# Kernel optimization log

Hardware: AMD Instinct MI355X
Metric: run time of the kernel (lower is better)

## Reference

```python
import jax, jax.numpy as jnp
import numpy as np

# --- static config (matches init_kwargs) ---
DIM = 192          # kv channels
CS = 2             # channel_scale -> q/out channels = DIM//CS
NH = 6             # num heads
WS = 4             # kv window size (q window = 2*WS)
S, H, W = 16, 32, 32          # coarse (input) resolution
SD, HD, WD = 32, 64, 64
HEAD = DIM // NH
SCALE = HEAD ** -0.5

# Relative position index: query coords are the fine-grid positions mapped to
# coarse coords via repeat_interleave(2) (as in the original coords_s/h/w),
# key coords are the coarse window positions. (Original torch code contained a
# buggy 2D->3D port of the strided key subsample; this is the consistent 3D form.)
_r = np.repeat(np.arange(WS), 2)
qc = np.stack(np.meshgrid(_r, _r, _r, indexing='ij'), -1).reshape(-1, 3)        # (512,3)
_k = np.arange(WS)
kc = np.stack(np.meshgrid(_k, _k, _k, indexing='ij'), -1).reshape(-1, 3)        # (64,3)
_rel = qc[:, None, :] - kc[None, :, :] + (WS - 1)                                # in [0, 2*WS-2]
REL_INDEX = jnp.asarray(_rel[..., 0] * (2 * WS - 1) ** 2 + _rel[..., 1] * (2 * WS - 1) + _rel[..., 2])  # (512,64)
TABLE_ROWS = (4 * WS - 1) ** 3  # as in original parameter shape


def ln(x, g, b, eps=1e-5):
    mu = jnp.mean(x, axis=-1, keepdims=True)
    var = jnp.mean(jnp.square(x - mu), axis=-1, keepdims=True)
    return (x - mu) * jax.lax.rsqrt(var + eps) * g + b


def win_part(x, ws):
    # (B,s,h,w,C) -> (B*num_windows, ws^3, C)
    B, s, h, w, C = x.shape
    x = x.reshape(B, s // ws, ws, h // ws, ws, w // ws, ws, C)
    return x.transpose(0, 1, 3, 5, 2, 4, 6, 7).reshape(-1, ws * ws * ws, C)


def win_rev(x, ws, B, s, h, w):
    # (B*num_windows, ws^3, C) -> (B,s,h,w,C)
    C = x.shape[-1]
    x = x.reshape(B, s // ws, h // ws, w // ws, ws, ws, ws, C)
    return x.transpose(0, 1, 4, 2, 5, 3, 6, 7).reshape(B, s, h, w, C)


def setup_inputs() -> dict:
    key = jax.random.key(0)
    ks = jax.random.split(key, 12)
    d = DIM
    dh = d // CS
    hid = int(dh * 4)
    f = lambda i, shape: jax.random.normal(ks[i], shape, jnp.float32) * 0.02
    return dict(
        x=jax.random.normal(ks[0], (2, S * H * W, d), jnp.float32),
        x_downsampled=jax.random.normal(ks[1], (2, SD * HD * WD, dh), jnp.float32),
        gamma1=jnp.ones((d,), jnp.float32), beta1=jnp.zeros((d,), jnp.float32),
        W_kv=f(2, (d, 2 * d)), b_kv=jnp.zeros((2 * d,), jnp.float32),
        W_q=f(3, (dh, d)), b_q=jnp.zeros((d,), jnp.float32),
        W_proj=f(4, (d, dh)), b_proj=jnp.zeros((dh,), jnp.float32),
        bias_table=f(5, (TABLE_ROWS, NH)),
        exp_gamma=jnp.ones((d,), jnp.float32), exp_beta=jnp.zeros((d,), jnp.float32),
        deconv_w=f(6, (d, dh, 2, 2, 2)), deconv_b=jnp.zeros((dh,), jnp.float32),
        gamma2=jnp.ones((dh,), jnp.float32), beta2=jnp.zeros((dh,), jnp.float32),
        W1=f(7, (dh, hid)), b1=jnp.zeros((hid,), jnp.float32),
        W2=f(8, (hid, dh)), b2=jnp.zeros((dh,), jnp.float32),
        padwh=0,
    )


def reference(x, x_downsampled, gamma1, beta1, W_kv, b_kv, W_q, b_q, W_proj, b_proj,
              bias_table, exp_gamma, exp_beta, deconv_w, deconv_b, gamma2, beta2,
              W1, b1, W2, b2, padwh):
    B = x.shape[0]
    d = DIM
    dh = d // CS
    # ---- windowed cross attention: kv from coarse x (norm1), q from fine skip ----
    kv = ln(x, gamma1, beta1).reshape(B, S, H, W, d)
    kv_w = win_part(kv, WS)                                           # (Bw, 64, d)
    q_w = win_part(x_downsampled.reshape(B, SD, HD, WD, dh), 2 * WS)  # (Bw, 512, dh)
    Bw, N, _ = kv_w.shape
    Nq = q_w.shape[1]
    kvp = kv_w @ W_kv + b_kv                                          # (Bw, N, 2d)
    k, v = jnp.split(kvp, 2, axis=-1)
    k = k.reshape(Bw, N, NH, HEAD).transpose(0, 2, 1, 3)
    v = v.reshape(Bw, N, NH, HEAD).transpose(0, 2, 1, 3)
    q = (q_w @ W_q + b_q).reshape(Bw, Nq, NH, HEAD).transpose(0, 2, 1, 3) * SCALE
    attn = jnp.einsum('bhqd,bhkd->bhqk', q, k)                        # (Bw, NH, 512, 64)
    bias = bias_table[REL_INDEX].transpose(2, 0, 1)                   # (NH, 512, 64)
    attn = jax.nn.softmax(attn + bias[None], axis=-1)
    out = jnp.einsum('bhqk,bhkd->bhqd', attn, v).transpose(0, 2, 1, 3).reshape(Bw, Nq, d)
    out = out @ W_proj + b_proj                                       # (Bw, Nq, dh)
    out = win_rev(out, 2 * WS, B, SD, HD, WD).reshape(B, SD * HD * WD, dh)
    # ---- Patch_Expanding residual: LN + ConvTranspose3d(k=2, s=2) ----
    xe = ln(x, exp_gamma, exp_beta).reshape(B, S, H, W, d)
    sc = jnp.einsum('bshwc,coijk->bsihjwko', xe, deconv_w) + deconv_b  # (B,S,2,H,2,W,2,dh)
    sc = sc.reshape(B, SD * HD * WD, dh)
    # ---- residual + MLP ----
    y = sc + out
    hdn = jax.nn.gelu(ln(y, gamma2, beta2) @ W1 + b1, approximate=False)
    return y + (hdn @ W2 + b2)
```

## Files before the change

### kernel.cpp

```cpp
#include <hip/hip_runtime.h>
#include <math.h>

#define ATT_SCALE 0.17677669529663687f

typedef __bf16 bf16x8 __attribute__((ext_vector_type(8)));
typedef __bf16 bf16x4 __attribute__((ext_vector_type(4)));
typedef float  f32x4  __attribute__((ext_vector_type(4)));

#define MFMA16(a,b,c) __builtin_amdgcn_mfma_f32_16x16x32_bf16(a,b,c,0,0,0)

#define BIAS_BYTES 786432
#define WKV_OFF 0
#define WQ_OFF  73728
#define WP_OFF  92160
#define WD_OFF  110592
#define W1_OFF  258048
#define W2_OFF  294912
#define NSWZ    331776

static __device__ __forceinline__ float gelu_exact(float v){
    return 0.5f * v * (1.0f + erff(v * 0.70710678118654752f));
}

static __device__ __forceinline__ bf16x8 afrag(const __bf16* w, int NRT, int kt, int rt, int lane){
    return ((const bf16x8*)w)[(kt*NRT + rt)*64 + lane];
}

__global__ __launch_bounds__(256) void k_prep(const float* __restrict__ table,
    const float* __restrict__ Wkv, const float* __restrict__ Wq,
    const float* __restrict__ Wp,  const float* __restrict__ Wd,
    const float* __restrict__ W1,  const float* __restrict__ W2,
    float* __restrict__ bias, __bf16* __restrict__ wsw){
    int id = blockIdx.x * 256 + threadIdx.x;
    if (id < 196608){
        int k  = id & 63;
        int qg = (id >> 6) & 511;
        int h  = id >> 15;
        int qi = qg >> 6, qj = (qg >> 3) & 7, qk = qg & 7;
        int ki = k >> 4,  kj = (k >> 2) & 3,  kk = k & 3;
        int r0 = (qi >> 1) - ki + 3;
        int r1 = (qj >> 1) - kj + 3;
        int r2 = (qk >> 1) - kk + 3;
        bias[id] = table[((r0 * 7 + r1) * 7 + r2) * 6 + h];
        return;
    }
    id -= 196608;
    if (id >= NSWZ) return;
    if (id >= WD_OFF && id < W1_OFF){
        int lid  = id - WD_OFF;
        int j    = lid & 7, lane = (lid >> 3) & 63, tile = lid >> 9;
        int rt   = tile % 24;
        int kt2  = tile / 24;
        int ii   = kt2 / 6, kt = kt2 % 6;
        int n    = rt * 16 + (lane & 15);
        int o    = n % 96, jk = n / 96;
        int kdim = kt * 32 + (lane >> 4) * 8 + j;
        wsw[id] = (__bf16)(Wd[(kdim * 96 + o) * 8 + ii * 4 + jk]);
        return;
    }
    const float* W; int N, NRT, off; float sc = 1.f;
    if      (id < WQ_OFF){ W = Wkv; N = 384; NRT = 24; off = WKV_OFF; }
    else if (id < WP_OFF){ W = Wq;  N = 192; NRT = 12; off = WQ_OFF; sc = ATT_SCALE; }
    else if (id < WD_OFF){ W = Wp;  N = 96;  NRT = 6;  off = WP_OFF; }
    else if (id < W2_OFF){ W = W1;  N = 384; NRT = 24; off = W1_OFF; }
    else                 { W = W2;  N = 96;  NRT = 6;  off = W2_OFF; }
    int lid  = id - off;
    int j    = lid & 7, lane = (lid >> 3) & 63, tile = lid >> 9;
    int rt   = tile % NRT, kt = tile / NRT;
    int n    = rt * 16 + (lane & 15);
    int k    = kt * 32 + (lane >> 4) * 8 + j;
    wsw[id + 0] = (__bf16)(W[k * N + n] * sc);
}

__global__ __launch_bounds__(512) void k_deconv(const float* __restrict__ x,
    const float* __restrict__ eg, const float* __restrict__ eb,
    const __bf16* __restrict__ wsw, const float* __restrict__ db,
    float* __restrict__ out){
    __shared__ __bf16 xe[64][200];
    const int tid = threadIdx.x, lane = tid & 63, w = tid >> 6;
    const int ci0 = blockIdx.x * 64;
    {
        int row = tid >> 3, sub = tid & 7;
        const float* xp = x + (ci0 + row) * 192 + sub * 24;
        float v[24]; float s = 0.f, ss = 0.f;
        #pragma unroll
        for (int i = 0; i < 6; i++){
            float4 t = ((const float4*)xp)[i];
            v[4*i] = t.x; v[4*i+1] = t.y; v[4*i+2] = t.z; v[4*i+3] = t.w;
            s += t.x + t.y + t.z + t.w;
            ss += t.x*t.x + t.y*t.y + t.z*t.z + t.w*t.w;
        }
        #pragma unroll
        for (int m = 1; m < 8; m <<= 1){ s += __shfl_xor(s, m); ss += __shfl_xor(ss, m); }
        float mu = s * (1.f/192.f), var = ss * (1.f/192.f) - mu*mu, rs = rsqrtf(var + 1e-5f);
        #pragma unroll
        for (int i = 0; i < 3; i++){
            bf16x8 t;
            #pragma unroll
            for (int jj = 0; jj < 8; jj++){
                int c = sub*24 + 8*i + jj;
                t[jj] = (__bf16)((v[8*i+jj] - mu) * rs * eg[c] + eb[c]);
            }
            *(bf16x8*)&xe[row][sub*24 + 8*i] = t;
        }
    }
    __syncthreads();
    const int li = lane & 15, gt = lane >> 4;
    const int ct = w & 3, ii = w >> 2;
    const int tok = ct * 16 + li;
    const int ci  = ci0 + tok;
    const int bb  = ci >> 14, rem = ci & 16383;
    const int sC  = rem >> 10, hC = (rem >> 5) & 31, wC = rem & 31;
    const int ftb = ((bb * 32 + 2 * sC) * 64 + 2 * hC) * 64 + 2 * wC + ii * 4096;
    bf16x8 bfr[6];
    #pragma unroll
    for (int kt = 0; kt < 6; kt++) bfr[kt] = *(const bf16x8*)&xe[tok][kt*32 + gt*8];
    const __bf16* wd = wsw + WD_OFF + ii * 73728;
    for (int rt = 0; rt < 24; rt++){
        f32x4 acc = {0.f,0.f,0.f,0.f};
        #pragma unroll
        for (int kt = 0; kt < 6; kt++) acc = MFMA16(afrag(wd, 24, kt, rt, lane), bfr[kt], acc);
        int m  = rt * 16 + (gt << 2);
        int jk = m / 96, o = m - jk * 96;
        int ft = ftb + (jk >> 1) * 64 + (jk & 1);
        float4 d4 = *(const float4*)&db[o];
        float4 res;
        res.x = acc[0] + d4.x; res.y = acc[1] + d4.y;
        res.z = acc[2] + d4.z; res.w = acc[3] + d4.w;
        *(float4*)&out[ft * 96 + o] = res;
    }
}

__global__ __launch_bounds__(512) void k_attn(const float* __restrict__ x,
    const float* __restrict__ xd, const float* __restrict__ g1, const float* __restrict__ b1v,
    const float* __restrict__ bkv, const float* __restrict__ bq, const float* __restrict__ bpj,
    const __bf16* __restrict__ wsw, const float* __restrict__ bias, float* __restrict__ yout){
    __shared__ __bf16 Qs[64][196];
    __shared__ __bf16 Ks[64][196];
    __shared__ __bf16 Vt[192][68];
    const int tid = threadIdx.x, lane = tid & 63, w = tid >> 6;
    const int win = blockIdx.x, b = win >> 8, wrem = win & 255;
    const int sw_ = wrem >> 6, hw_ = (wrem >> 3) & 7, ww_ = wrem & 7;

    {
        int row = tid >> 3, sub = tid & 7;
        int si = row >> 4, hi = (row >> 2) & 3, wi = row & 3;
        int ci = ((b * 16 + 4 * sw_ + si) * 32 + 4 * hw_ + hi) * 32 + 4 * ww_ + wi;
        const float* xp = x + ci * 192 + sub * 24;
        float v[24]; float s = 0.f, ss = 0.f;
        #pragma unroll
        for (int i = 0; i < 6; i++){
            float4 t = ((const float4*)xp)[i];
            v[4*i] = t.x; v[4*i+1] = t.y; v[4*i+2] = t.z; v[4*i+3] = t.w;
            s += t.x + t.y + t.z + t.w;
            ss += t.x*t.x + t.y*t.y + t.z*t.z + t.w*t.w;
        }
        #pragma unroll
        for (int m = 1; m < 8; m <<= 1){ s += __shfl_xor(s, m); ss += __shfl_xor(ss, m); }
        float mu = s * (1.f/192.f), var = ss * (1.f/192.f) - mu*mu, rs = rsqrtf(var + 1e-5f);
        #pragma unroll
        for (int i = 0; i < 3; i++){
            bf16x8 t;
            #pragma unroll
            for (int jj = 0; jj < 8; jj++){
                int c = sub*24 + 8*i + jj;
                t[jj] = (__bf16)((v[8*i+jj] - mu) * rs * g1[c] + b1v[c]);
            }
            *(bf16x8*)&Qs[row][sub*24 + 8*i] = t;
        }
    }
    __syncthreads();
    {
        const int ct = w & 3, rh = w >> 2;
        const int tok = ct * 16 + (lane & 15);
        bf16x8 bfr[6];
        #pragma unroll
        for (int kt = 0; kt < 6; kt++) bfr[kt] = *(const bf16x8*)&Qs[tok][kt*32 + (lane>>4)*8];
        #pragma unroll
        for (int i = 0; i < 12; i++){
            int rt = rh * 12 + i;
            f32x4 acc = {0.f,0.f,0.f,0.f};
            #pragma unroll
            for (int kt = 0; kt < 6; kt++) acc = MFMA16(afrag(wsw + WKV_OFF, 24, kt, rt, lane), bfr[kt], acc);
            int cb = rt * 16 + ((lane >> 4) << 2);
            float4 b4 = *(const float4*)&bkv[cb];
            acc[0] += b4.x; acc[1] += b4.y; acc[2] += b4.z; acc[3] += b4.w;
            if (cb < 192){
                bf16x4 t;
                #pragma unroll
                for (int r = 0; r < 4; r++) t[r] = (__bf16)acc[r];
                *(bf16x4*)&Ks[tok][cb] = t;
            } else {
                #pragma unroll
                for (int r = 0; r < 4; r++) Vt[cb - 192 + r][tok] = (__bf16)acc[r];
            }
        }
    }
    __syncthreads();

    const int li_ = lane & 15, gt_ = lane >> 4, rsel = lane >> 5;

    for (int qt = 0; qt < 8; qt++){
        {
            const int ct = w & 3, rh = w >> 2;
            const int ql = ct * 16 + (lane & 15);
            const int ft = ((b * 32 + 8 * sw_ + qt) * 64 + 8 * hw_ + (ql >> 3)) * 64 + 8 * ww_ + (ql & 7);
            bf16x8 bfr[3];
            #pragma unroll
            for (int kt = 0; kt < 3; kt++){
                const float* xp = xd + ft * 96 + kt * 32 + (lane >> 4) * 8;
                float4 t0 = *(const float4*)xp;
                float4 t1 = *(const float4*)(xp + 4);
                bf16x8 t;
                t[0]=(__bf16)t0.x; t[1]=(__bf16)t0.y; t[2]=(__bf16)t0.z; t[3]=(__bf16)t0.w;
                t[4]=(__bf16)t1.x; t[5]=(__bf16)t1.y; t[6]=(__bf16)t1.z; t[7]=(__bf16)t1.w;
                bfr[kt] = t;
            }
            #pragma unroll
            for (int i = 0; i < 6; i++){
                int rt = rh * 6 + i;
                f32x4 acc = {0.f,0.f,0.f,0.f};
                #pragma unroll
                for (int kt = 0; kt < 3; kt++) acc = MFMA16(afrag(wsw + WQ_OFF, 12, kt, rt, lane), bfr[kt], acc);
                int cb = rt * 16 + ((lane >> 4) << 2);
                float4 b4 = *(const float4*)&bq[cb];
                bf16x4 t;
                t[0] = (__bf16)(acc[0] + b4.x * ATT_SCALE);
                t[1] = (__bf16)(acc[1] + b4.y * ATT_SCALE);
                t[2] = (__bf16)(acc[2] + b4.z * ATT_SCALE);
                t[3] = (__bf16)(acc[3] + b4.w * ATT_SCALE);
                *(bf16x4*)&Qs[ql][cb] = t;
            }
        }
        __syncthreads();
        f32x4 ov[3][2];
        #pragma unroll
        for (int ui = 0; ui < 3; ui++){
            const int u = w * 3 + ui;
            const int h = u >> 2, qct = u & 3;
            f32x4 sc[4];
            __builtin_amdgcn_s_setprio(1);
            #pragma unroll
            for (int rt = 0; rt < 4; rt++){
                bf16x8 a  = *(const bf16x8*)&Ks[rt*16 + li_][h*32 + gt_*8];
                bf16x8 bq8 = *(const bf16x8*)&Qs[qct*16 + li_][h*32 + gt_*8];
                f32x4 z = {0.f,0.f,0.f,0.f};
                sc[rt] = MFMA16(a, bq8, z);
            }
            __builtin_amdgcn_s_setprio(0);
            const int qg = qt * 64 + qct * 16 + li_;
            const float* bp = bias + (h * 512 + qg) * 64 + (gt_ << 2);
            #pragma unroll
            for (int rt = 0; rt < 4; rt++){
                float4 b4 = *(const float4*)(bp + rt * 16);
                sc[rt][0] += b4.x; sc[rt][1] += b4.y; sc[rt][2] += b4.z; sc[rt][3] += b4.w;
            }
            float m = sc[0][0];
            #pragma unroll
            for (int rt = 0; rt < 4; rt++)
                #pragma unroll
                for (int r = 0; r < 4; r++) m = fmaxf(m, sc[rt][r]);
            m = fmaxf(m, __shfl_xor(m, 16));
            m = fmaxf(m, __shfl_xor(m, 32));
            float sum = 0.f;
            #pragma unroll
            for (int rt = 0; rt < 4; rt++)
                #pragma unroll
                for (int r = 0; r < 4; r++){ float e = __expf(sc[rt][r] - m); sc[rt][r] = e; sum += e; }
            sum += __shfl_xor(sum, 16);
            sum += __shfl_xor(sum, 32);
            float inv = 1.f / sum;
            unsigned pwv[4][2];
            #pragma unroll
            for (int rt = 0; rt < 4; rt++){
                union { __bf16 hh[2]; unsigned u; } c0, c1;
                c0.hh[0] = (__bf16)(sc[rt][0] * inv); c0.hh[1] = (__bf16)(sc[rt][1] * inv);
                c1.hh[0] = (__bf16)(sc[rt][2] * inv); c1.hh[1] = (__bf16)(sc[rt][3] * inv);
                pwv[rt][0] = c0.u; pwv[rt][1] = c1.u;
            }
            unsigned bfw[2][4];
            #pragma unroll
            for (int kt = 0; kt < 2; kt++){
                #pragma unroll
                for (int t = 0; t < 4; t++){
                    int gs   = ((gt_ & 1) << 1) + (t >> 1);
                    int addr = (((gs << 4) + li_) << 2);
                    int w0 = __builtin_amdgcn_ds_bpermute(addr, (int)pwv[2*kt + 0][t & 1]);
                    int w1 = __builtin_amdgcn_ds_bpermute(addr, (int)pwv[2*kt + 1][t & 1]);
                    bfw[kt][t] = rsel ? (unsigned)w1 : (unsigned)w0;
                }
            }
            union { unsigned u[4]; bf16x8 v; } pb0, pb1;
            #pragma unroll
            for (int t = 0; t < 4; t++){ pb0.u[t] = bfw[0][t]; pb1.u[t] = bfw[1][t]; }
            __builtin_amdgcn_s_setprio(1);
            #pragma unroll
            for (int dt = 0; dt < 2; dt++){
                f32x4 o = {0.f,0.f,0.f,0.f};
                bf16x8 a0 = *(const bf16x8*)&Vt[h*32 + dt*16 + li_][gt_*8];
                bf16x8 a1 = *(const bf16x8*)&Vt[h*32 + dt*16 + li_][32 + gt_*8];
                o = MFMA16(a0, pb0.v, o);
                o = MFMA16(a1, pb1.v, o);
                ov[ui][dt] = o;
            }
            __builtin_amdgcn_s_setprio(0);
        }
        __syncthreads();
        #pragma unroll
        for (int ui = 0; ui < 3; ui++){
            const int u = w * 3 + ui;
            const int h = u >> 2, qct = u & 3;
            const int tok = qct * 16 + li_;
            #pragma unroll
            for (int dt = 0; dt < 2; dt++){
                int cb = h * 32 + dt * 16 + (gt_ << 2);
                bf16x4 t;
                #pragma unroll
                for (int r = 0; r < 4; r++) t[r] = (__bf16)ov[ui][dt][r];
                *(bf16x4*)&Qs[tok][cb] = t;
            }
        }
        __syncthreads();
        {
            const int ct = w & 3, rh = w >> 2;
            const int ql = ct * 16 + (lane & 15);
            const int ft = ((b * 32 + 8 * sw_ + qt) * 64 + 8 * hw_ + (ql >> 3)) * 64 + 8 * ww_ + (ql & 7);
            bf16x8 bfr[6];
            #pragma unroll
            for (int kt = 0; kt < 6; kt++) bfr[kt] = *(const bf16x8*)&Qs[ql][kt*32 + (lane>>4)*8];
            #pragma unroll
            for (int i = 0; i < 3; i++){
                int rt = rh * 3 + i;
                f32x4 acc = {0.f,0.f,0.f,0.f};
                #pragma unroll
                for (int kt = 0; kt < 6; kt++) acc = MFMA16(afrag(wsw + WP_OFF, 6, kt, rt, lane), bfr[kt], acc);
                int cb = rt * 16 + ((lane >> 4) << 2);
                float4 b4 = *(const float4*)&bpj[cb];
                float4 old = *(const float4*)&yout[ft * 96 + cb];
                float4 res;
                res.x = old.x + acc[0] + b4.x;
                res.y = old.y + acc[1] + b4.y;
                res.z = old.z + acc[2] + b4.z;
                res.w = old.w + acc[3] + b4.w;
                *(float4*)&yout[ft * 96 + cb] = res;
            }
        }
        __syncthreads();
    }
}

__global__ __launch_bounds__(512) void k_mlp(const float* __restrict__ y,
    const float* __restrict__ g2, const float* __restrict__ b2v,
    const __bf16* __restrict__ wsw, const float* __restrict__ b1m,
    const float* __restrict__ b2m, float* __restrict__ outp){
    __shared__ __bf16 yln[64][104];
    __shared__ __bf16 hsm[64][200];
    __shared__ __bf16 ybf[64][96];
    const int tid = threadIdx.x, lane = tid & 63, w = tid >> 6;
    const int t0 = blockIdx.x * 64;
    {
        int row = tid >> 3, sub = tid & 7;
        const float* yp = y + (t0 + row) * 96 + sub * 12;
        float v[12]; float s = 0.f, ss = 0.f;
        #pragma unroll
        for (int i = 0; i < 3; i++){
            float4 t = ((const float4*)yp)[i];
            v[4*i] = t.x; v[4*i+1] = t.y; v[4*i+2] = t.z; v[4*i+3] = t.w;
            s += t.x + t.y + t.z + t.w;
            ss += t.x*t.x + t.y*t.y + t.z*t.z + t.w*t.w;
        }
        #pragma unroll
        for (int i = 0; i < 3; i++){
            bf16x4 t;
            #pragma unroll
            for (int jj = 0; jj < 4; jj++) t[jj] = (__bf16)v[4*i+jj];
            *(bf16x4*)&ybf[row][sub*12 + 4*i] = t;
        }
        #pragma unroll
        for (int m = 1; m < 8; m <<= 1){ s += __shfl_xor(s, m); ss += __shfl_xor(ss, m); }
        float mu = s * (1.f/96.f), var = ss * (1.f/96.f) - mu*mu, rs = rsqrtf(var + 1e-5f);
        #pragma unroll
        for (int i = 0; i < 3; i++){
            bf16x4 t;
            #pragma unroll
            for (int jj = 0; jj < 4; jj++){
                int c = sub*12 + 4*i + jj;
                t[jj] = (__bf16)((v[4*i+jj] - mu) * rs * g2[c] + b2v[c]);
            }
            *(bf16x4*)&yln[row][sub*12 + 4*i] = t;
        }
    }
    __syncthreads();
    const int ct = w & 3, rh = w >> 2;
    const int tok = ct * 16 + (lane & 15);
    bf16x8 bfrY[3];
    #pragma unroll
    for (int kt = 0; kt < 3; kt++) bfrY[kt] = *(const bf16x8*)&yln[tok][kt*32 + (lane>>4)*8];
    f32x4 oacc[3];
    #pragma unroll
    for (int i = 0; i < 3; i++){ f32x4 z = {0.f,0.f,0.f,0.f}; oacc[i] = z; }

    #pragma unroll
    for (int hh = 0; hh < 2; hh++){
        #pragma unroll
        for (int i = 0; i < 6; i++){
            int rtl = rh * 6 + i;
            int rtg = hh * 12 + rtl;
            f32x4 acc = {0.f,0.f,0.f,0.f};
            #pragma unroll
            for (int kt = 0; kt < 3; kt++) acc = MFMA16(afrag(wsw + W1_OFF, 24, kt, rtg, lane), bfrY[kt], acc);
            int cb = rtl * 16 + ((lane >> 4) << 2);
            float4 b4 = *(const float4*)&b1m[hh * 192 + cb];
            bf16x4 t;
            t[0] = (__bf16)gelu_exact(acc[0] + b4.x);
            t[1] = (__bf16)gelu_exact(acc[1] + b4.y);
            t[2] = (__bf16)gelu_exact(acc[2] + b4.z);
            t[3] = (__bf16)gelu_exact(acc[3] + b4.w);
            *(bf16x4*)&hsm[tok][cb] = t;
        }
        __syncthreads();
        bf16x8 bfrH[6];
        #pragma unroll
        for (int kt = 0; kt < 6; kt++) bfrH[kt] = *(const bf16x8*)&hsm[tok][kt*32 + (lane>>4)*8];
        #pragma unroll
        for (int i = 0; i < 3; i++){
            int rt = rh * 3 + i;
            #pragma unroll
            for (int kt = 0; kt < 6; kt++)
                oacc[i] = MFMA16(afrag(wsw + W2_OFF, 6, hh * 6 + kt, rt, lane), bfrH[kt], oacc[i]);
        }
        __syncthreads();
    }
    #pragma unroll
    for (int i = 0; i < 3; i++){
        int rt = rh * 3 + i;
        int cb = rt * 16 + ((lane >> 4) << 2);
        float4 b4 = *(const float4*)&b2m[cb];
        bf16x4 yv = *(const bf16x4*)&ybf[tok][cb];
        float4 res;
        res.x = (float)yv[0] + oacc[i][0] + b4.x;
        res.y = (float)yv[1] + oacc[i][1] + b4.y;
        res.z = (float)yv[2] + oacc[i][2] + b4.z;
        res.w = (float)yv[3] + oacc[i][3] + b4.w;
        *(float4*)&outp[(t0 + tok) * 96 + cb] = res;
    }
}

extern "C" void kernel_launch(void* const* d_in, const int* in_sizes, int n_in,
                              void* d_out, int out_size, void* d_ws, size_t ws_size,
                              hipStream_t stream){
    const float* x    = (const float*)d_in[0];
    const float* xd   = (const float*)d_in[1];
    const float* g1   = (const float*)d_in[2];
    const float* b1v  = (const float*)d_in[3];
    const float* Wkv  = (const float*)d_in[4];
    const float* bkv  = (const float*)d_in[5];
    const float* Wq   = (const float*)d_in[6];
    const float* bq   = (const float*)d_in[7];
    const float* Wp   = (const float*)d_in[8];
    const float* bpj  = (const float*)d_in[9];
    const float* btab = (const float*)d_in[10];
    const float* eg   = (const float*)d_in[11];
    const float* eb   = (const float*)d_in[12];
    const float* dw   = (const float*)d_in[13];
    const float* db   = (const float*)d_in[14];
    const float* g2   = (const float*)d_in[15];
    const float* b2v  = (const float*)d_in[16];
    const float* W1   = (const float*)d_in[17];
    const float* b1m  = (const float*)d_in[18];
    const float* W2   = (const float*)d_in[19];
    const float* b2m  = (const float*)d_in[20];
    (void)in_sizes; (void)n_in; (void)out_size; (void)ws_size;

    float*   out  = (float*)d_out;
    float*   bias = (float*)d_ws;
    __bf16*  wsw  = (__bf16*)((char*)d_ws + BIAS_BYTES);

    k_prep  <<<2064, 256, 0, stream>>>(btab, Wkv, Wq, Wp, dw, W1, W2, bias, wsw);
    k_deconv<<<512, 512, 0, stream>>>(x, eg, eb, wsw, db, out);
    k_attn  <<<512, 512, 0, stream>>>(x, xd, g1, b1v, bkv, bq, bpj, wsw, bias, out);
    k_mlp   <<<4096, 512, 0, stream>>>(out, g2, b2v, wsw, b1m, b2m, out);
}
```

Baseline: 320.8 us.

## Fuse patch-expanding deconv residual into MLP kernel, drop separate deconv pass

Removes the standalone deconvolution kernel. Each MLP block now recomputes LayerNorm plus the ConvTranspose3d for the 32 coarse tokens feeding its 64 fine tokens, and adds the result to the attention output in shared memory. The attention kernel now writes its projection directly instead of read-modify-writing the output buffer. This cuts a full write and read of the 25 MB fp32 intermediate and one kernel launch, at the cost of more shared memory per MLP block (which may lower occupancy) and extra work inside the MLP kernel. The residual y is also kept in fp32 rather than bf16.

```diff
diff --git a/kernel.cpp b/kernel.cpp
--- a/kernel.cpp
+++ b/kernel.cpp
@@ -72,65 +72,6 @@
     wsw[id + 0] = (__bf16)(W[k * N + n] * sc);
 }
 
-__global__ __launch_bounds__(512) void k_deconv(const float* __restrict__ x,
-    const float* __restrict__ eg, const float* __restrict__ eb,
-    const __bf16* __restrict__ wsw, const float* __restrict__ db,
-    float* __restrict__ out){
-    __shared__ __bf16 xe[64][200];
-    const int tid = threadIdx.x, lane = tid & 63, w = tid >> 6;
-    const int ci0 = blockIdx.x * 64;
-    {
-        int row = tid >> 3, sub = tid & 7;
-        const float* xp = x + (ci0 + row) * 192 + sub * 24;
-        float v[24]; float s = 0.f, ss = 0.f;
-        #pragma unroll
-        for (int i = 0; i < 6; i++){
-            float4 t = ((const float4*)xp)[i];
-            v[4*i] = t.x; v[4*i+1] = t.y; v[4*i+2] = t.z; v[4*i+3] = t.w;
-            s += t.x + t.y + t.z + t.w;
-            ss += t.x*t.x + t.y*t.y + t.z*t.z + t.w*t.w;
-        }
-        #pragma unroll
-        for (int m = 1; m < 8; m <<= 1){ s += __shfl_xor(s, m); ss += __shfl_xor(ss, m); }
-        float mu = s * (1.f/192.f), var = ss * (1.f/192.f) - mu*mu, rs = rsqrtf(var + 1e-5f);
-        #pragma unroll
-        for (int i = 0; i < 3; i++){
-            bf16x8 t;
-            #pragma unroll
-            for (int jj = 0; jj < 8; jj++){
-                int c = sub*24 + 8*i + jj;
-                t[jj] = (__bf16)((v[8*i+jj] - mu) * rs * eg[c] + eb[c]);
-            }
-            *(bf16x8*)&xe[row][sub*24 + 8*i] = t;
-        }
-    }
-    __syncthreads();
-    const int li = lane & 15, gt = lane >> 4;
-    const int ct = w & 3, ii = w >> 2;
-    const int tok = ct * 16 + li;
-    const int ci  = ci0 + tok;
-    const int bb  = ci >> 14, rem = ci & 16383;
-    const int sC  = rem >> 10, hC = (rem >> 5) & 31, wC = rem & 31;
-    const int ftb = ((bb * 32 + 2 * sC) * 64 + 2 * hC) * 64 + 2 * wC + ii * 4096;
-    bf16x8 bfr[6];
-    #pragma unroll
-    for (int kt = 0; kt < 6; kt++) bfr[kt] = *(const bf16x8*)&xe[tok][kt*32 + gt*8];
-    const __bf16* wd = wsw + WD_OFF + ii * 73728;
-    for (int rt = 0; rt < 24; rt++){
-        f32x4 acc = {0.f,0.f,0.f,0.f};
-        #pragma unroll
-        for (int kt = 0; kt < 6; kt++) acc = MFMA16(afrag(wd, 24, kt, rt, lane), bfr[kt], acc);
-        int m  = rt * 16 + (gt << 2);
-        int jk = m / 96, o = m - jk * 96;
-        int ft = ftb + (jk >> 1) * 64 + (jk & 1);
-        float4 d4 = *(const float4*)&db[o];
-        float4 res;
-        res.x = acc[0] + d4.x; res.y = acc[1] + d4.y;
-        res.z = acc[2] + d4.z; res.w = acc[3] + d4.w;
-        *(float4*)&out[ft * 96 + o] = res;
-    }
-}
-
 __global__ __launch_bounds__(512) void k_attn(const float* __restrict__ x,
     const float* __restrict__ xd, const float* __restrict__ g1, const float* __restrict__ b1v,
     const float* __restrict__ bkv, const float* __restrict__ bq, const float* __restrict__ bpj,
@@ -336,12 +277,11 @@
                 for (int kt = 0; kt < 6; kt++) acc = MFMA16(afrag(wsw + WP_OFF, 6, kt, rt, lane), bfr[kt], acc);
                 int cb = rt * 16 + ((lane >> 4) << 2);
                 float4 b4 = *(const float4*)&bpj[cb];
-                float4 old = *(const float4*)&yout[ft * 96 + cb];
                 float4 res;
-                res.x = old.x + acc[0] + b4.x;
-                res.y = old.y + acc[1] + b4.y;
-                res.z = old.z + acc[2] + b4.z;
-                res.w = old.w + acc[3] + b4.w;
+                res.x = acc[0] + b4.x;
+                res.y = acc[1] + b4.y;
+                res.z = acc[2] + b4.z;
+                res.w = acc[3] + b4.w;
                 *(float4*)&yout[ft * 96 + cb] = res;
             }
         }
@@ -349,45 +289,104 @@
     }
 }
 
-__global__ __launch_bounds__(512) void k_mlp(const float* __restrict__ y,
+__global__ __launch_bounds__(512) void k_mlp(const float* __restrict__ x,
+    const float* __restrict__ eg, const float* __restrict__ eb,
     const float* __restrict__ g2, const float* __restrict__ b2v,
-    const __bf16* __restrict__ wsw, const float* __restrict__ b1m,
-    const float* __restrict__ b2m, float* __restrict__ outp){
+    const __bf16* __restrict__ wsw, const float* __restrict__ db,
+    const float* __restrict__ b1m, const float* __restrict__ b2m,
+    float* __restrict__ outp){
+    __shared__ __bf16 xe[32][200];
+    __shared__ float  ysl[64][100];
     __shared__ __bf16 yln[64][104];
     __shared__ __bf16 hsm[64][200];
-    __shared__ __bf16 ybf[64][96];
     const int tid = threadIdx.x, lane = tid & 63, w = tid >> 6;
     const int t0 = blockIdx.x * 64;
+    const int bb   = t0 >> 17;
+    const int sbar = (t0 >> 12) & 31;
+    const int hbar = (t0 >> 6) & 63;
+    const int iD = sbar & 1, jD = hbar & 1;
+    const int sc_ = sbar >> 1, hc_ = hbar >> 1;
+
+    {
+        int row = tid >> 4, sub = tid & 15;
+        int ci = ((bb * 16 + sc_) * 32 + hc_) * 32 + row;
+        const float* xp = x + ci * 192 + sub * 12;
+        float v[12]; float s = 0.f, ss = 0.f;
+        #pragma unroll
+        for (int i2 = 0; i2 < 3; i2++){
+            float4 t = ((const float4*)xp)[i2];
+            v[4*i2] = t.x; v[4*i2+1] = t.y; v[4*i2+2] = t.z; v[4*i2+3] = t.w;
+            s += t.x + t.y + t.z + t.w;
+            ss += t.x*t.x + t.y*t.y + t.z*t.z + t.w*t.w;
+        }
+        #pragma unroll
+        for (int m = 1; m < 16; m <<= 1){ s += __shfl_xor(s, m); ss += __shfl_xor(ss, m); }
+        float mu = s * (1.f/192.f), var = ss * (1.f/192.f) - mu*mu, rs = rsqrtf(var + 1e-5f);
+        #pragma unroll
+        for (int i2 = 0; i2 < 3; i2++){
+            bf16x4 t;
+            #pragma unroll
+            for (int jj = 0; jj < 4; jj++){
+                int c = sub*12 + 4*i2 + jj;
+                t[jj] = (__bf16)((v[4*i2+jj] - mu) * rs * eg[c] + eb[c]);
+            }
+            *(bf16x4*)&xe[row][sub*12 + 4*i2] = t;
+        }
+    }
+    __syncthreads();
+    {
+        const int li = lane & 15, gt = lane >> 4;
+        const int ctD = w & 1, rhD = w >> 1;
+        const int wcol = ctD * 16 + li;
+        bf16x8 bfrD[6];
+        #pragma unroll
+        for (int kt = 0; kt < 6; kt++) bfrD[kt] = *(const bf16x8*)&xe[wcol][kt*32 + gt*8];
+        const __bf16* wd = wsw + WD_OFF + iD * 73728;
+        #pragma unroll
+        for (int i2 = 0; i2 < 3; i2++){
+            int rtl = rhD * 3 + i2;
+            int rt  = 12 * jD + rtl;
+            f32x4 acc = {0.f,0.f,0.f,0.f};
+            #pragma unroll
+            for (int kt = 0; kt < 6; kt++) acc = MFMA16(afrag(wd, 24, kt, rt, lane), bfrD[kt], acc);
+            int mp   = rtl * 16 + (gt << 2);
+            int kpar = (mp >= 96) ? 1 : 0;
+            int o    = mp - 96 * kpar;
+            int tok  = 2 * wcol + kpar;
+            float4 d4 = *(const float4*)&db[o];
+            float4 res;
+            res.x = acc[0] + d4.x; res.y = acc[1] + d4.y;
+            res.z = acc[2] + d4.z; res.w = acc[3] + d4.w;
+            *(float4*)&ysl[tok][o] = res;
+        }
+    }
+    __syncthreads();
     {
         int row = tid >> 3, sub = tid & 7;
-        const float* yp = y + (t0 + row) * 96 + sub * 12;
+        const float* ap = outp + (t0 + row) * 96 + sub * 12;
         float v[12]; float s = 0.f, ss = 0.f;
         #pragma unroll
-        for (int i = 0; i < 3; i++){
-            float4 t = ((const float4*)yp)[i];
-            v[4*i] = t.x; v[4*i+1] = t.y; v[4*i+2] = t.z; v[4*i+3] = t.w;
+        for (int i2 = 0; i2 < 3; i2++){
+            float4 t = ((const float4*)ap)[i2];
+            float4 s4 = *(const float4*)&ysl[row][sub*12 + 4*i2];
+            t.x += s4.x; t.y += s4.y; t.z += s4.z; t.w += s4.w;
+            v[4*i2] = t.x; v[4*i2+1] = t.y; v[4*i2+2] = t.z; v[4*i2+3] = t.w;
             s += t.x + t.y + t.z + t.w;
             ss += t.x*t.x + t.y*t.y + t.z*t.z + t.w*t.w;
-        }
-        #pragma unroll
-        for (int i = 0; i < 3; i++){
-            bf16x4 t;
-            #pragma unroll
-            for (int jj = 0; jj < 4; jj++) t[jj] = (__bf16)v[4*i+jj];
-            *(bf16x4*)&ybf[row][sub*12 + 4*i] = t;
+            *(float4*)&ysl[row][sub*12 + 4*i2] = t;
         }
         #pragma unroll
         for (int m = 1; m < 8; m <<= 1){ s += __shfl_xor(s, m); ss += __shfl_xor(ss, m); }
         float mu = s * (1.f/96.f), var = ss * (1.f/96.f) - mu*mu, rs = rsqrtf(var + 1e-5f);
         #pragma unroll
-        for (int i = 0; i < 3; i++){
+        for (int i2 = 0; i2 < 3; i2++){
             bf16x4 t;
             #pragma unroll
             for (int jj = 0; jj < 4; jj++){
-                int c = sub*12 + 4*i + jj;
-                t[jj] = (__bf16)((v[4*i+jj] - mu) * rs * g2[c] + b2v[c]);
-            }
-            *(bf16x4*)&yln[row][sub*12 + 4*i] = t;
+                int c = sub*12 + 4*i2 + jj;
+                t[jj] = (__bf16)((v[4*i2+jj] - mu) * rs * g2[c] + b2v[c]);
+            }
+            *(bf16x4*)&yln[row][sub*12 + 4*i2] = t;
         }
     }
     __syncthreads();
@@ -436,12 +435,12 @@
         int rt = rh * 3 + i;
         int cb = rt * 16 + ((lane >> 4) << 2);
         float4 b4 = *(const float4*)&b2m[cb];
-        bf16x4 yv = *(const bf16x4*)&ybf[tok][cb];
+        float4 yv = *(const float4*)&ysl[tok][cb];
         float4 res;
-        res.x = (float)yv[0] + oacc[i][0] + b4.x;
-        res.y = (float)yv[1] + oacc[i][1] + b4.y;
-        res.z = (float)yv[2] + oacc[i][2] + b4.z;
-        res.w = (float)yv[3] + oacc[i][3] + b4.w;
+        res.x = yv.x + oacc[i][0] + b4.x;
+        res.y = yv.y + oacc[i][1] + b4.y;
+        res.z = yv.z + oacc[i][2] + b4.z;
+        res.w = yv.w + oacc[i][3] + b4.w;
         *(float4*)&outp[(t0 + tok) * 96 + cb] = res;
     }
 }
@@ -476,8 +475,7 @@
     float*   bias = (float*)d_ws;
     __bf16*  wsw  = (__bf16*)((char*)d_ws + BIAS_BYTES);
 
-    k_prep  <<<2064, 256, 0, stream>>>(btab, Wkv, Wq, Wp, dw, W1, W2, bias, wsw);
-    k_deconv<<<512, 512, 0, stream>>>(x, eg, eb, wsw, db, out);
-    k_attn  <<<512, 512, 0, stream>>>(x, xd, g1, b1v, bkv, bq, bpj, wsw, bias, out);
-    k_mlp   <<<4096, 512, 0, stream>>>(out, g2, b2v, wsw, b1m, b2m, out);
-}
+    k_prep<<<2064, 256, 0, stream>>>(btab, Wkv, Wq, Wp, dw, W1, W2, bias, wsw);
+    k_attn<<<512, 512, 0, stream>>>(x, xd, g1, b1v, bkv, bq, bpj, wsw, bias, out);
+    k_mlp <<<4096, 512, 0, stream>>>(x, eg, eb, g2, b2v, wsw, db, b1m, b2m, out);
+}
```

After: 305.1 us. 1.05x faster.
